# Optimization experiments

Hardware: AMD Instinct MI355X
Metric: run time of the kernel (lower is better)

Reference implementation:

```python
import jax, jax.numpy as jnp
import numpy as np

N_CELLS = 50000
HID = 64
DEG = 16
K_NODES = 4  # nodes per cell; cell i owns nodes [4i, 4i+4)
SP = 3


def setup_inputs() -> dict:
    key = jax.random.key(0)
    ks = jax.random.split(key, 12)
    s = 1.0 / np.sqrt(HID)
    inp = {
        'features': jax.random.normal(ks[0], (N_CELLS, HID), jnp.float32),
        'positions': jax.random.normal(ks[1], (K_NODES * N_CELLS, SP), jnp.float32),
        'neighbors': jax.random.randint(ks[2], (N_CELLS, DEG), 0, N_CELLS, jnp.int32),
        # message MLP: Linear(2H+1 -> H), SiLU, Linear(H -> H)
        'W1': jax.random.normal(ks[3], (2 * HID + 1, HID), jnp.float32) * s,
        'b1': jnp.zeros((HID,), jnp.float32),
        'W2': jax.random.normal(ks[4], (HID, HID), jnp.float32) * s,
        'b2': jnp.zeros((HID,), jnp.float32),
        # update MLP: Linear(H + H -> H), SiLU, Linear(H -> H)
        'Wu1': jax.random.normal(ks[5], (2 * HID, HID), jnp.float32) * s,
        'bu1': jnp.zeros((HID,), jnp.float32),
        'Wu2': jax.random.normal(ks[6], (HID, HID), jnp.float32) * s,
        'bu2': jnp.zeros((HID,), jnp.float32),
    }
    return inp


def reference(features, positions, neighbors, W1, b1, W2, b2, Wu1, bu1, Wu2, bu2):
    N, H = features.shape
    # centroid of each cell's owned nodes (cell i -> nodes [K*i, K*i+K))
    cent = positions.reshape(N, K_NODES, SP).mean(axis=1)          # [N, sp]
    fj = features[neighbors]                                       # [N, D, H]
    cj = cent[neighbors]                                           # [N, D, sp]
    # centroid-distance geometric invariant per (cell, neighbor) pair
    geom = jnp.linalg.norm(cent[:, None, :] - cj, axis=-1, keepdims=True)  # [N, D, 1]
    fi = jnp.broadcast_to(features[:, None, :], fj.shape)          # [N, D, H]
    x = jnp.concatenate([fi, fj, geom], axis=-1)                   # [N, D, 2H+1]
    h = jax.nn.silu(x @ W1 + b1) @ W2 + b2                         # [N, D, H]
    msg = h.mean(axis=1)                                           # mean over neighbors
    u = jnp.concatenate([features, msg], axis=-1)                  # [N, 2H]
    upd = jax.nn.silu(u @ Wu1 + bu1) @ Wu2 + bu2
    updated_features = features + upd
    return updated_features, positions
```

## Files before the change

### kernel.cpp

```cpp
#include <hip/hip_runtime.h>


#define DEG 16

typedef __attribute__((ext_vector_type(8))) short short8;
typedef __attribute__((ext_vector_type(4))) float f32x4;
typedef uint2 uint2_a __attribute__((may_alias));
typedef uint4 uint4_a __attribute__((may_alias));
typedef unsigned short ushort_a __attribute__((may_alias));

union HbRd { uint4_a u; short8 s; };
union Frag { short8 s; uint4 u; };

__device__ __forceinline__ unsigned f2bf(float f) {
  unsigned u = __float_as_uint(f);
  return (u + 0x7FFFu + ((u >> 16) & 1u)) >> 16;
}
__device__ __forceinline__ float bf2f(unsigned bits16) {
  return __uint_as_float(bits16 << 16);
}
__device__ __forceinline__ float silu(float h) {
  return h / (1.f + __expf(-h));
}
__device__ __forceinline__ float silu_fast(float h) {
  return h * __builtin_amdgcn_rcpf(1.f + __expf(-h));
}

#define EARLY_LOADS(T, NJ, G, XF)                                              \
  {                                                                            \
    _Pragma("unroll")                                                          \
    for (int i_ = 0; i_ < 4; ++i_) {                                           \
      const int cs_ = __builtin_amdgcn_readfirstlane((T) * 16 + wid * 4 + i_); \
      NJ[i_] = nbr[cs_ * DEG + l15];                                           \
    }                                                                          \
    _Pragma("unroll")                                                          \
    for (int i_ = 0; i_ < 4; ++i_) {                                           \
      const int cs_ = __builtin_amdgcn_readfirstlane((T) * 16 + wid * 4 + i_); \
      const float4 ci_ = cent4c[cs_];                                          \
      const float4 cj_ = cent4c[NJ[i_]];                                       \
      const float dx_ = ci_.x - cj_.x, dy_ = ci_.y - cj_.y,                    \
                  dz_ = ci_.z - cj_.z;                                         \
      G[i_] = sqrtf(dx_ * dx_ + dy_ * dy_ + dz_ * dz_);                        \
    }                                                                          \
    const int crE_ = (T) * 16 + l15;                                           \
    _Pragma("unroll")                                                          \
    for (int kk_ = 0; kk_ < 2; ++kk_) {                                        \
      const float4 f0_ =                                                       \
          *(const float4*)(feat + crE_ * 64 + kk_ * 32 + quad * 8);            \
      const float4 f1_ =                                                       \
          *(const float4*)(feat + crE_ * 64 + kk_ * 32 + quad * 8 + 4);        \
      Frag v_;                                                                 \
      v_.s[0] = (short)f2bf(f0_.x); v_.s[1] = (short)f2bf(f0_.y);              \
      v_.s[2] = (short)f2bf(f0_.z); v_.s[3] = (short)f2bf(f0_.w);              \
      v_.s[4] = (short)f2bf(f1_.x); v_.s[5] = (short)f2bf(f1_.y);              \
      v_.s[6] = (short)f2bf(f1_.z); v_.s[7] = (short)f2bf(f1_.w);              \
      XF[kk_] = v_.s;                                                          \
    }                                                                          \
  }

__global__ __launch_bounds__(256) void prep_aux_kernel(
    const float* __restrict__ feat,
    const float* __restrict__ pos,
    const float* __restrict__ W1, const float* __restrict__ W2,
    const float* __restrict__ Wu1, const float* __restrict__ Wu2,
    float* __restrict__ outpos, float* __restrict__ cent4,
    unsigned short* __restrict__ w1pq, unsigned short* __restrict__ w2t,
    unsigned short* __restrict__ wu1t, unsigned short* __restrict__ wu2b,
    unsigned char* __restrict__ Q8)
{
  __shared__ unsigned short w1q[4096];

  if (blockIdx.x < 782) {
    const int tid  = threadIdx.x;
    const int lane = tid & 63;
    const int wid  = tid >> 6;
    const int quad = lane >> 4;
    const int l15  = lane & 15;

    {
      const int q  = (tid >> 3) & 3;
      const int kk = (tid >> 5) & 1;
      const int mq = tid >> 6;
      #pragma unroll
      for (int u = 0; u < 2; ++u) {
        const int l = (tid * 2 + u) & 15;
        const float* src = W1 + (64 + kk * 32 + q * 8) * 64 + mq * 16 + l;
        unsigned short v[8];
        #pragma unroll
        for (int j = 0; j < 8; ++j)
          v[j] = (unsigned short)f2bf(src[j * 64]);
        uint4 pk;
        pk.x = (unsigned)v[0] | ((unsigned)v[1] << 16);
        pk.y = (unsigned)v[2] | ((unsigned)v[3] << 16);
        pk.z = (unsigned)v[4] | ((unsigned)v[5] << 16);
        pk.w = (unsigned)v[6] | ((unsigned)v[7] << 16);
        ((uint4*)w1q)[tid * 2 + u] = pk;
      }
    }

    const int tile = blockIdx.x * 4 + wid;
    const bool act = (tile < 3125);
    const int  tt  = act ? tile : 3124;
    const int  cr  = tt * 16 + l15;

    short8 xf[2];
    #pragma unroll
    for (int kk = 0; kk < 2; ++kk) {
      const float4 f0 = *(const float4*)(feat + cr * 64 + kk * 32 + quad * 8);
      const float4 f1 = *(const float4*)(feat + cr * 64 + kk * 32 + quad * 8 + 4);
      Frag v;
      v.s[0] = (short)f2bf(f0.x); v.s[1] = (short)f2bf(f0.y);
      v.s[2] = (short)f2bf(f0.z); v.s[3] = (short)f2bf(f0.w);
      v.s[4] = (short)f2bf(f1.x); v.s[5] = (short)f2bf(f1.y);
      v.s[6] = (short)f2bf(f1.z); v.s[7] = (short)f2bf(f1.w);
      xf[kk] = v.s;
    }

    __syncthreads();

    short8 wf[4][2];
    #pragma unroll
    for (int m = 0; m < 4; ++m)
      #pragma unroll
      for (int kk = 0; kk < 2; ++kk)
        wf[m][kk] = *(const short8*)(w1q + (((m * 2 + kk) * 4 + quad) << 7) + l15 * 8);

    f32x4 acc[4] = {};
    #pragma unroll
    for (int kk = 0; kk < 2; ++kk)
      #pragma unroll
      for (int m = 0; m < 4; ++m)
        acc[m] = __builtin_amdgcn_mfma_f32_16x16x32_bf16(wf[m][kk], xf[kk], acc[m], 0, 0, 0);

    if (act) {
      #pragma unroll
      for (int m = 0; m < 4; ++m) {
        int w = __builtin_amdgcn_cvt_pk_fp8_f32(acc[m][0], acc[m][1], 0, false);
        w = __builtin_amdgcn_cvt_pk_fp8_f32(acc[m][2], acc[m][3], w, true);
        *(unsigned int*)(Q8 + cr * 64 + m * 16 + quad * 4) = (unsigned)w;
      }
    }
  } else {
    const int t = (blockIdx.x - 782) * 256 + threadIdx.x;
    if (t < 150000) {
      ((float4*)outpos)[t] = ((const float4*)pos)[t];
    } else if (t < 174576) {
      const int r = t - 150000;
      if (r < 8192) {
        const int j = r & 7, l = (r >> 3) & 15, q = (r >> 7) & 3;
        const int f = r >> 9, kk = f & 1, mt = f >> 1;
        const int k = kk * 32 + q * 8 + j;
        const int m = mt * 16 + l;
        w1pq[r] = (unsigned short)f2bf(
            (m < 64) ? W1[k * 64 + m] : W1[(k + 64) * 64 + (m - 64)]);
      } else if (r < 12288) {
        const int s = r - 8192;
        const int j = s & 7, l = (s >> 3) & 15, q = (s >> 7) & 3;
        const int f = s >> 9, kk = f & 1, mt = f >> 1;
        const int k = kk * 32 + q * 8 + j;
        w2t[s] = (unsigned short)f2bf(W2[k * 64 + mt * 16 + l]);
      } else if (r < 20480) {
        const int s = r - 12288;
        const int j = s & 7, l = (s >> 3) & 15, q = (s >> 7) & 3;
        const int f = s >> 9, kk = f & 3, mt = f >> 2;
        const int k = kk * 32 + q * 8 + j;
        wu1t[s] = (unsigned short)f2bf(Wu1[k * 64 + mt * 16 + l]);
      } else {
        const int s = r - 20480;
        const int j = s & 7, l = (s >> 3) & 15, q = (s >> 7) & 3;
        const int f = s >> 9, kk = f & 1, nt = f >> 1;
        const int k = kk * 32 + q * 8 + j;
        wu2b[s] = (unsigned short)f2bf(Wu2[k * 64 + nt * 16 + l]);
      }
    } else if (t < 224576) {
      const int i = t - 174576;
      const float4* pp = (const float4*)(pos + 12 * i);
      const float4 a = pp[0], b = pp[1], c = pp[2];
      float4 o;
      o.x = (a.x + a.w + b.z + c.y) * 0.25f;
      o.y = (a.y + b.x + b.w + c.z) * 0.25f;
      o.z = (a.z + b.y + c.x + c.w) * 0.25f;
      o.w = 0.f;
      ((float4*)cent4)[i] = o;
    }
  }
}

__global__ __launch_bounds__(256) void msg_tail_kernel(
    const unsigned char* __restrict__ Q8,
    const float4* __restrict__ cent4c,
    const int* __restrict__ nbr,
    const float* __restrict__ feat,
    const unsigned short* __restrict__ w1pq,
    const unsigned short* __restrict__ w2t,
    const unsigned short* __restrict__ wu1t,
    const unsigned short* __restrict__ wu2b,
    const float* __restrict__ b1, const float* __restrict__ W1,
    const float* __restrict__ b2, const float* __restrict__ bu1,
    const float* __restrict__ bu2,
    float* __restrict__ outf)
{
  __shared__ uint4 smem[432];
  char* sT  = (char*)smem;
  char* Msg = sT + 2304;
  char* Hb  = sT + 4608;

  const int lane = threadIdx.x & 63;
  const int wid  = threadIdx.x >> 6;
  const int quad = lane >> 4;
  const int l15  = lane & 15;
  const int bid  = blockIdx.x;
  const int gdim = gridDim.x;

  const float b1l = b1[lane];
  const float wl  = W1[8192 + lane];

  short8 wpf[2], w2f[2], wu1f[4], wu2f[2];
  #pragma unroll
  for (int kk = 0; kk < 2; ++kk)
    wpf[kk]  = *(const short8*)(w1pq + (((wid * 2 + kk) * 4 + quad) << 7) + l15 * 8);
  #pragma unroll
  for (int kk = 0; kk < 2; ++kk)
    w2f[kk]  = *(const short8*)(w2t  + (((wid * 2 + kk) * 4 + quad) << 7) + l15 * 8);
  #pragma unroll
  for (int kk = 0; kk < 4; ++kk)
    wu1f[kk] = *(const short8*)(wu1t + (((wid * 4 + kk) * 4 + quad) << 7) + l15 * 8);
  #pragma unroll
  for (int kk = 0; kk < 2; ++kk)
    wu2f[kk] = *(const short8*)(wu2b + (((wid * 2 + kk) * 4 + quad) << 7) + l15 * 8);

  const f32x4 b2f  = *(const f32x4*)(b2  + wid * 16 + quad * 4);
  const f32x4 bu1f = *(const f32x4*)(bu1 + wid * 16 + quad * 4);
  const float bu2v = bu2[wid * 16 + l15];

  int nj[4]; float g[4]; short8 xf[2];
  EARLY_LOADS(bid, nj, g, xf);

  for (int tile = bid; tile < 3125; tile += gdim) {
    {
      f32x4 accp = {};
      #pragma unroll
      for (int kk = 0; kk < 2; ++kk)
        accp = __builtin_amdgcn_mfma_f32_16x16x32_bf16(wpf[kk], xf[kk], accp, 0, 0, 0);
      uint2 pk;
      pk.x = f2bf(accp[0]) | (f2bf(accp[1]) << 16);
      pk.y = f2bf(accp[2]) | (f2bf(accp[3]) << 16);
      *(uint2_a*)(sT + l15 * 144 + wid * 32 + quad * 8) = pk;
    }

    unsigned qA[16], qB[16];
    #pragma unroll
    for (int d = 0; d < 16; ++d) {
      const int nd = __builtin_amdgcn_readlane(nj[0], d);
      qA[d] = Q8[nd * 64 + lane];
    }

    __syncthreads();

    #pragma unroll
    for (int i = 0; i < 4; ++i) {
      unsigned (&qc)[16] = (i & 1) ? qB : qA;
      unsigned (&qn)[16] = (i & 1) ? qA : qB;
      if (i < 3) {
        #pragma unroll
        for (int d = 0; d < 16; ++d) {
          const int nd = __builtin_amdgcn_readlane(nj[i + 1], d);
          qn[d] = Q8[nd * 64 + lane];
        }
      }
      const float pcb =
          bf2f(((const ushort_a*)(sT + (wid * 4 + i) * 144))[lane]) + b1l;
      float acc = 0.f;
      #pragma unroll
      for (int d = 0; d < 16; ++d) {
        const float gd = __uint_as_float(
            __builtin_amdgcn_readlane((int)__float_as_uint(g[i]), d));
        const float qv = __builtin_amdgcn_cvt_f32_fp8((int)qc[d], 0);
        acc += silu_fast(pcb + qv + gd * wl);
      }
      ((ushort_a*)(sT + (wid * 4 + i) * 144))[lane] =
          (unsigned short)f2bf(acc * 0.0625f);
    }

    __syncthreads();

    int nj2[4]; float g2[4]; short8 xf2[2];
    const int tn = tile + gdim;
    if (tn < 3125) EARLY_LOADS(tn, nj2, g2, xf2);

    {
      f32x4 accm = {};
      #pragma unroll
      for (int kk = 0; kk < 2; ++kk) {
        HbRd t; t.u = *(const uint4_a*)(sT + l15 * 144 + kk * 64 + quad * 16);
        accm = __builtin_amdgcn_mfma_f32_16x16x32_bf16(w2f[kk], t.s, accm, 0, 0, 0);
      }
      uint2 pk;
      pk.x = f2bf(accm[0] + b2f[0]) | (f2bf(accm[1] + b2f[1]) << 16);
      pk.y = f2bf(accm[2] + b2f[2]) | (f2bf(accm[3] + b2f[3]) << 16);
      *(uint2_a*)(Msg + l15 * 144 + wid * 32 + quad * 8) = pk;
    }
    __syncthreads();

    {
      f32x4 accu = {};
      #pragma unroll
      for (int kk = 0; kk < 4; ++kk) {
        short8 bf;
        if (kk < 2) {
          bf = xf[kk];
        } else {
          HbRd t; t.u = *(const uint4_a*)(Msg + l15 * 144 + (kk - 2) * 64 + quad * 16);
          bf = t.s;
        }
        accu = __builtin_amdgcn_mfma_f32_16x16x32_bf16(wu1f[kk], bf, accu, 0, 0, 0);
      }
      float sv[4];
      #pragma unroll
      for (int rg = 0; rg < 4; ++rg)
        sv[rg] = silu(accu[rg] + bu1f[rg]);
      uint2 pk;
      pk.x = f2bf(sv[0]) | (f2bf(sv[1]) << 16);
      pk.y = f2bf(sv[2]) | (f2bf(sv[3]) << 16);
      *(uint2_a*)(Hb + l15 * 144 + wid * 32 + quad * 8) = pk;
    }
    __syncthreads();

    {
      f32x4 acc2 = {};
      #pragma unroll
      for (int kk = 0; kk < 2; ++kk) {
        HbRd t; t.u = *(const uint4_a*)(Hb + l15 * 144 + kk * 64 + quad * 16);
        acc2 = __builtin_amdgcn_mfma_f32_16x16x32_bf16(t.s, wu2f[kk], acc2, 0, 0, 0);
      }
      #pragma unroll
      for (int rg = 0; rg < 4; ++rg) {
        const int row = tile * 16 + quad * 4 + rg;
        const int col = wid * 16 + l15;
        outf[row * 64 + col] = feat[row * 64 + col] + acc2[rg] + bu2v;
      }
    }

    if (tn < 3125) {
      #pragma unroll
      for (int i = 0; i < 4; ++i) { nj[i] = nj2[i]; g[i] = g2[i]; }
      xf[0] = xf2[0]; xf[1] = xf2[1];
    }
  }
}

extern "C" void kernel_launch(void* const* d_in, const int* in_sizes, int n_in,
                              void* d_out, int out_size, void* d_ws, size_t ws_size,
                              hipStream_t stream)
{
  const float* feat = (const float*)d_in[0];
  const float* pos  = (const float*)d_in[1];
  const int*   nbr  = (const int*)d_in[2];
  const float* W1   = (const float*)d_in[3];
  const float* b1   = (const float*)d_in[4];
  const float* W2   = (const float*)d_in[5];
  const float* b2   = (const float*)d_in[6];
  const float* Wu1  = (const float*)d_in[7];
  const float* bu1  = (const float*)d_in[8];
  const float* Wu2  = (const float*)d_in[9];
  const float* bu2  = (const float*)d_in[10];
  float* out = (float*)d_out;

  unsigned char*  Q8    = (unsigned char*)((char*)d_ws + 12800000);
  float*          cent4 = (float*)((char*)d_ws + 25600000);
  unsigned short* w1pq  = (unsigned short*)((char*)d_ws + 26400000);
  unsigned short* w2t   = (unsigned short*)((char*)d_ws + 26416384);
  unsigned short* wu1t  = (unsigned short*)((char*)d_ws + 26424576);
  unsigned short* wu2b  = (unsigned short*)((char*)d_ws + 26440960);

  prep_aux_kernel<<<1660, 256, 0, stream>>>(feat, pos, W1, W2, Wu1, Wu2,
                                            out + 3200000, cent4,
                                            w1pq, w2t, wu1t, wu2b, Q8);
  msg_tail_kernel<<<1042, 256, 0, stream>>>(Q8, (const float4*)cent4, nbr, feat,
                                            w1pq, w2t, wu1t, wu2b,
                                            b1, W1, b2, bu1, bu2, out);
}
```

Baseline: 132.6 us.

## Replace persistent tile loop with one block per tile and deeper gather prefetch

The message/update kernel drops its grid-stride persistent loop and launches one block per 16-cell tile (3125 blocks). Gathers for two neighbor groups are issued before the projection MFMA, and each finished buffer is refilled with the group two ahead. The prep kernel's W1 bf16 staging is also rewritten to read W1 with coalesced float4 loads and scatter into LDS. The goal is more blocks in flight to hide gather latency, at the cost of reloading per-block weight fragments 3125 times instead of 1042.

```diff
diff --git a/kernel.cpp b/kernel.cpp
--- a/kernel.cpp
+++ b/kernel.cpp
@@ -78,23 +78,18 @@
     const int l15  = lane & 15;
 
     {
-      const int q  = (tid >> 3) & 3;
-      const int kk = (tid >> 5) & 1;
-      const int mq = tid >> 6;
-      #pragma unroll
-      for (int u = 0; u < 2; ++u) {
-        const int l = (tid * 2 + u) & 15;
-        const float* src = W1 + (64 + kk * 32 + q * 8) * 64 + mq * 16 + l;
-        unsigned short v[8];
-        #pragma unroll
-        for (int j = 0; j < 8; ++j)
-          v[j] = (unsigned short)f2bf(src[j * 64]);
-        uint4 pk;
-        pk.x = (unsigned)v[0] | ((unsigned)v[1] << 16);
-        pk.y = (unsigned)v[2] | ((unsigned)v[3] << 16);
-        pk.z = (unsigned)v[4] | ((unsigned)v[5] << 16);
-        pk.w = (unsigned)v[6] | ((unsigned)v[7] << 16);
-        ((uint4*)w1q)[tid * 2 + u] = pk;
+      const int k  = tid >> 2;
+      const int mq = tid & 3;
+      const int kk = k >> 5, q = (k >> 3) & 3, j = k & 7;
+      const int sbase = ((mq * 2 + kk) * 4 + q) * 128 + j;
+      const float* src = W1 + 4096 + tid * 16;
+      #pragma unroll
+      for (int c = 0; c < 4; ++c) {
+        const float4 f = *(const float4*)(src + c * 4);
+        w1q[sbase + (c * 4 + 0) * 8] = (unsigned short)f2bf(f.x);
+        w1q[sbase + (c * 4 + 1) * 8] = (unsigned short)f2bf(f.y);
+        w1q[sbase + (c * 4 + 2) * 8] = (unsigned short)f2bf(f.z);
+        w1q[sbase + (c * 4 + 3) * 8] = (unsigned short)f2bf(f.w);
       }
     }
 
@@ -209,8 +204,8 @@
   const int wid  = threadIdx.x >> 6;
   const int quad = lane >> 4;
   const int l15  = lane & 15;
-  const int bid  = blockIdx.x;
-  const int gdim = gridDim.x;
+  const int tile = blockIdx.x;
+  const int cr   = tile * 16 + l15;
 
   const float b1l = b1[lane];
   const float wl  = W1[8192 + lane];
@@ -234,117 +229,109 @@
   const float bu2v = bu2[wid * 16 + l15];
 
   int nj[4]; float g[4]; short8 xf[2];
-  EARLY_LOADS(bid, nj, g, xf);
-
-  for (int tile = bid; tile < 3125; tile += gdim) {
-    {
-      f32x4 accp = {};
-      #pragma unroll
-      for (int kk = 0; kk < 2; ++kk)
-        accp = __builtin_amdgcn_mfma_f32_16x16x32_bf16(wpf[kk], xf[kk], accp, 0, 0, 0);
-      uint2 pk;
-      pk.x = f2bf(accp[0]) | (f2bf(accp[1]) << 16);
-      pk.y = f2bf(accp[2]) | (f2bf(accp[3]) << 16);
-      *(uint2_a*)(sT + l15 * 144 + wid * 32 + quad * 8) = pk;
-    }
-
-    unsigned qA[16], qB[16];
+  EARLY_LOADS(tile, nj, g, xf);
+
+  unsigned qA[16], qB[16];
+  #pragma unroll
+  for (int d = 0; d < 16; ++d) {
+    const int nd = __builtin_amdgcn_readlane(nj[0], d);
+    qA[d] = Q8[nd * 64 + lane];
+  }
+  #pragma unroll
+  for (int d = 0; d < 16; ++d) {
+    const int nd = __builtin_amdgcn_readlane(nj[1], d);
+    qB[d] = Q8[nd * 64 + lane];
+  }
+
+  {
+    f32x4 accp = {};
+    #pragma unroll
+    for (int kk = 0; kk < 2; ++kk)
+      accp = __builtin_amdgcn_mfma_f32_16x16x32_bf16(wpf[kk], xf[kk], accp, 0, 0, 0);
+    uint2 pk;
+    pk.x = f2bf(accp[0]) | (f2bf(accp[1]) << 16);
+    pk.y = f2bf(accp[2]) | (f2bf(accp[3]) << 16);
+    *(uint2_a*)(sT + l15 * 144 + wid * 32 + quad * 8) = pk;
+  }
+
+  __syncthreads();
+
+  #pragma unroll
+  for (int i = 0; i < 4; ++i) {
+    unsigned (&qc)[16] = (i & 1) ? qB : qA;
+    const float pcb =
+        bf2f(((const ushort_a*)(sT + (wid * 4 + i) * 144))[lane]) + b1l;
+    float acc = 0.f;
     #pragma unroll
     for (int d = 0; d < 16; ++d) {
-      const int nd = __builtin_amdgcn_readlane(nj[0], d);
-      qA[d] = Q8[nd * 64 + lane];
-    }
-
-    __syncthreads();
-
-    #pragma unroll
-    for (int i = 0; i < 4; ++i) {
-      unsigned (&qc)[16] = (i & 1) ? qB : qA;
-      unsigned (&qn)[16] = (i & 1) ? qA : qB;
-      if (i < 3) {
-        #pragma unroll
-        for (int d = 0; d < 16; ++d) {
-          const int nd = __builtin_amdgcn_readlane(nj[i + 1], d);
-          qn[d] = Q8[nd * 64 + lane];
-        }
-      }
-      const float pcb =
-          bf2f(((const ushort_a*)(sT + (wid * 4 + i) * 144))[lane]) + b1l;
-      float acc = 0.f;
+      const float gd = __uint_as_float(
+          __builtin_amdgcn_readlane((int)__float_as_uint(g[i]), d));
+      const float qv = __builtin_amdgcn_cvt_f32_fp8((int)qc[d], 0);
+      acc += silu_fast(pcb + qv + gd * wl);
+    }
+    if (i < 2) {
       #pragma unroll
       for (int d = 0; d < 16; ++d) {
-        const float gd = __uint_as_float(
-            __builtin_amdgcn_readlane((int)__float_as_uint(g[i]), d));
-        const float qv = __builtin_amdgcn_cvt_f32_fp8((int)qc[d], 0);
-        acc += silu_fast(pcb + qv + gd * wl);
-      }
-      ((ushort_a*)(sT + (wid * 4 + i) * 144))[lane] =
-          (unsigned short)f2bf(acc * 0.0625f);
-    }
-
-    __syncthreads();
-
-    int nj2[4]; float g2[4]; short8 xf2[2];
-    const int tn = tile + gdim;
-    if (tn < 3125) EARLY_LOADS(tn, nj2, g2, xf2);
-
-    {
-      f32x4 accm = {};
-      #pragma unroll
-      for (int kk = 0; kk < 2; ++kk) {
-        HbRd t; t.u = *(const uint4_a*)(sT + l15 * 144 + kk * 64 + quad * 16);
-        accm = __builtin_amdgcn_mfma_f32_16x16x32_bf16(w2f[kk], t.s, accm, 0, 0, 0);
-      }
-      uint2 pk;
-      pk.x = f2bf(accm[0] + b2f[0]) | (f2bf(accm[1] + b2f[1]) << 16);
-      pk.y = f2bf(accm[2] + b2f[2]) | (f2bf(accm[3] + b2f[3]) << 16);
-      *(uint2_a*)(Msg + l15 * 144 + wid * 32 + quad * 8) = pk;
-    }
-    __syncthreads();
-
-    {
-      f32x4 accu = {};
-      #pragma unroll
-      for (int kk = 0; kk < 4; ++kk) {
-        short8 bf;
-        if (kk < 2) {
-          bf = xf[kk];
-        } else {
-          HbRd t; t.u = *(const uint4_a*)(Msg + l15 * 144 + (kk - 2) * 64 + quad * 16);
-          bf = t.s;
-        }
-        accu = __builtin_amdgcn_mfma_f32_16x16x32_bf16(wu1f[kk], bf, accu, 0, 0, 0);
-      }
-      float sv[4];
-      #pragma unroll
-      for (int rg = 0; rg < 4; ++rg)
-        sv[rg] = silu(accu[rg] + bu1f[rg]);
-      uint2 pk;
-      pk.x = f2bf(sv[0]) | (f2bf(sv[1]) << 16);
-      pk.y = f2bf(sv[2]) | (f2bf(sv[3]) << 16);
-      *(uint2_a*)(Hb + l15 * 144 + wid * 32 + quad * 8) = pk;
-    }
-    __syncthreads();
-
-    {
-      f32x4 acc2 = {};
-      #pragma unroll
-      for (int kk = 0; kk < 2; ++kk) {
-        HbRd t; t.u = *(const uint4_a*)(Hb + l15 * 144 + kk * 64 + quad * 16);
-        acc2 = __builtin_amdgcn_mfma_f32_16x16x32_bf16(t.s, wu2f[kk], acc2, 0, 0, 0);
-      }
-      #pragma unroll
-      for (int rg = 0; rg < 4; ++rg) {
-        const int row = tile * 16 + quad * 4 + rg;
-        const int col = wid * 16 + l15;
-        outf[row * 64 + col] = feat[row * 64 + col] + acc2[rg] + bu2v;
-      }
-    }
-
-    if (tn < 3125) {
-      #pragma unroll
-      for (int i = 0; i < 4; ++i) { nj[i] = nj2[i]; g[i] = g2[i]; }
-      xf[0] = xf2[0]; xf[1] = xf2[1];
+        const int nd = __builtin_amdgcn_readlane(nj[i + 2], d);
+        qc[d] = Q8[nd * 64 + lane];
+      }
+    }
+    ((ushort_a*)(sT + (wid * 4 + i) * 144))[lane] =
+        (unsigned short)f2bf(acc * 0.0625f);
+  }
+
+  __syncthreads();
+
+  {
+    f32x4 accm = {};
+    #pragma unroll
+    for (int kk = 0; kk < 2; ++kk) {
+      HbRd t; t.u = *(const uint4_a*)(sT + l15 * 144 + kk * 64 + quad * 16);
+      accm = __builtin_amdgcn_mfma_f32_16x16x32_bf16(w2f[kk], t.s, accm, 0, 0, 0);
+    }
+    uint2 pk;
+    pk.x = f2bf(accm[0] + b2f[0]) | (f2bf(accm[1] + b2f[1]) << 16);
+    pk.y = f2bf(accm[2] + b2f[2]) | (f2bf(accm[3] + b2f[3]) << 16);
+    *(uint2_a*)(Msg + l15 * 144 + wid * 32 + quad * 8) = pk;
+  }
+  __syncthreads();
+
+  {
+    f32x4 accu = {};
+    #pragma unroll
+    for (int kk = 0; kk < 4; ++kk) {
+      short8 bf;
+      if (kk < 2) {
+        bf = xf[kk];
+      } else {
+        HbRd t; t.u = *(const uint4_a*)(Msg + l15 * 144 + (kk - 2) * 64 + quad * 16);
+        bf = t.s;
+      }
+      accu = __builtin_amdgcn_mfma_f32_16x16x32_bf16(wu1f[kk], bf, accu, 0, 0, 0);
+    }
+    float sv[4];
+    #pragma unroll
+    for (int rg = 0; rg < 4; ++rg)
+      sv[rg] = silu(accu[rg] + bu1f[rg]);
+    uint2 pk;
+    pk.x = f2bf(sv[0]) | (f2bf(sv[1]) << 16);
+    pk.y = f2bf(sv[2]) | (f2bf(sv[3]) << 16);
+    *(uint2_a*)(Hb + l15 * 144 + wid * 32 + quad * 8) = pk;
+  }
+  __syncthreads();
+
+  {
+    f32x4 acc2 = {};
+    #pragma unroll
+    for (int kk = 0; kk < 2; ++kk) {
+      HbRd t; t.u = *(const uint4_a*)(Hb + l15 * 144 + kk * 64 + quad * 16);
+      acc2 = __builtin_amdgcn_mfma_f32_16x16x32_bf16(t.s, wu2f[kk], acc2, 0, 0, 0);
+    }
+    #pragma unroll
+    for (int rg = 0; rg < 4; ++rg) {
+      const int row = tile * 16 + quad * 4 + rg;
+      const int col = wid * 16 + l15;
+      outf[row * 64 + col] = feat[row * 64 + col] + acc2[rg] + bu2v;
     }
   }
 }
@@ -376,7 +363,7 @@
   prep_aux_kernel<<<1660, 256, 0, stream>>>(feat, pos, W1, W2, Wu1, Wu2,
                                             out + 3200000, cent4,
                                             w1pq, w2t, wu1t, wu2b, Q8);
-  msg_tail_kernel<<<1042, 256, 0, stream>>>(Q8, (const float4*)cent4, nbr, feat,
+  msg_tail_kernel<<<3125, 256, 0, stream>>>(Q8, (const float4*)cent4, nbr, feat,
                                             w1pq, w2t, wu1t, wu2b,
                                             b1, W1, b2, bu1, bu2, out);
 }
```

After: 122.4 us. 7.7% less time.
